# Kernel optimization log

Hardware: AMD Instinct MI355X
Metric: run time of the kernel (lower is better)

Reference implementation:

```python
import jax, jax.numpy as jnp
import numpy as np

N = 16384
D_IN = 1024
HID = [512, 512, 256]
N_PAIRS = 100000
N_CLS = 3


def setup_inputs() -> dict:
    key = jax.random.key(0)
    ks = jax.random.split(key, 16)
    x = jax.random.normal(ks[0], (N, D_IN), dtype=jnp.float32)
    adj = jax.random.uniform(ks[1], (N, N), dtype=jnp.float32) / N  # dense normalized adjacency
    tf_idx = jax.random.randint(ks[2], (N_PAIRS,), 0, N)
    gene_idx = jax.random.randint(ks[3], (N_PAIRS,), 0, N)
    # GCN layer weights
    W0 = jax.random.normal(ks[4], (D_IN, HID[0]), dtype=jnp.float32) / np.sqrt(D_IN)
    b0 = jnp.zeros((HID[0],), dtype=jnp.float32)
    W1 = jax.random.normal(ks[5], (HID[0], HID[1]), dtype=jnp.float32) / np.sqrt(HID[0])
    b1 = jnp.zeros((HID[1],), dtype=jnp.float32)
    W2 = jax.random.normal(ks[6], (HID[1], HID[2]), dtype=jnp.float32) / np.sqrt(HID[1])
    b2 = jnp.zeros((HID[2],), dtype=jnp.float32)
    # MLP head: Linear(2*256 -> 256), GELU, Linear(256 -> 3)
    Wh1 = jax.random.normal(ks[7], (2 * HID[2], HID[2]), dtype=jnp.float32) / np.sqrt(2 * HID[2])
    bh1 = jnp.zeros((HID[2],), dtype=jnp.float32)
    Wh2 = jax.random.normal(ks[8], (HID[2], N_CLS), dtype=jnp.float32) / np.sqrt(HID[2])
    bh2 = jnp.zeros((N_CLS,), dtype=jnp.float32)
    return {"x": x, "adj": adj, "tf_idx": tf_idx, "gene_idx": gene_idx,
            "W0": W0, "b0": b0, "W1": W1, "b1": b1, "W2": W2, "b2": b2,
            "Wh1": Wh1, "bh1": bh1, "Wh2": Wh2, "bh2": bh2}


def reference(x, adj, tf_idx, gene_idx, W0, b0, W1, b1, W2, b2, Wh1, bh1, Wh2, bh2):
    # GCNConv: out = adj @ (x @ W) + b; ReLU between layers (dropout off in eval)
    h = jax.nn.relu(adj @ (x @ W0) + b0)          # [N, 512]
    h = jax.nn.relu(adj @ (h @ W1) + b1)          # [N, 512]
    emb = adj @ (h @ W2) + b2                      # [N, 256]
    pair = jnp.concatenate([emb[tf_idx], emb[gene_idx]], axis=-1)  # [P, 512]
    hdn = jax.nn.gelu(pair @ Wh1 + bh1, approximate=False)          # [P, 256]
    logits = hdn @ Wh2 + bh2                                        # [P, 3]
    return logits
```

## Files before the change

kernel.cpp:

```cpp
#include <hip/hip_runtime.h>
#include <hip/hip_bf16.h>
#include <stdint.h>


using f32x4  = __attribute__((ext_vector_type(4))) float;
using bf16x8 = __attribute__((ext_vector_type(8))) __bf16;
using u16x8  = __attribute__((ext_vector_type(8))) unsigned short;
using u16x4  = __attribute__((ext_vector_type(4))) unsigned short;

static __device__ __forceinline__ unsigned short f2bf(float f) {
  unsigned u = __builtin_bit_cast(unsigned, f);
  u += 0x7FFFu + ((u >> 16) & 1u);
  return (unsigned short)(u >> 16);
}
static __device__ __forceinline__ float bf2f(unsigned short h) {
  unsigned u = ((unsigned)h) << 16;
  return __builtin_bit_cast(float, u);
}
static __device__ __forceinline__ void gload_lds16(const void* g, void* l) {
  __builtin_amdgcn_global_load_lds((__attribute__((address_space(1))) void*)(void*)g,
                                   (__attribute__((address_space(3))) void*)l,
                                   16, 0, 0);
}


__global__ void tcvt_kernel(const float* __restrict__ in,
                            unsigned short* __restrict__ outp, int K, int Nf) {
  int id = blockIdx.x * 256 + threadIdx.x;
  if (id >= K * Nf) return;
  int k = id % K, nf = id / K;
  outp[id] = f2bf(in[(size_t)k * Nf + nf]);
}

__global__ void cvt_bf16_kernel(const float* __restrict__ in,
                                unsigned short* __restrict__ outp, size_t n) {
  size_t i = ((size_t)blockIdx.x * blockDim.x + threadIdx.x) * 8;
  size_t stride = (size_t)gridDim.x * blockDim.x * 8;
  for (; i + 8 <= n; i += stride) {
    const float4* p = (const float4*)(in + i);
    float4 a = p[0], b = p[1];
    u16x8 v;
    v[0] = f2bf(a.x); v[1] = f2bf(a.y); v[2] = f2bf(a.z); v[3] = f2bf(a.w);
    v[4] = f2bf(b.x); v[5] = f2bf(b.y); v[6] = f2bf(b.z); v[7] = f2bf(b.w);
    *(u16x8*)(outp + i) = v;
  }
}

__global__ void reduce2_kernel(const float* __restrict__ Pp, const float* __restrict__ bias,
                               unsigned short* __restrict__ outp, int MN, int Nf) {
  int i = (blockIdx.x * 256 + threadIdx.x) * 4;
  if (i >= MN) return;
  float4 a = *(const float4*)(Pp + i);
  float4 b = *(const float4*)(Pp + MN + i);
  int col = i & (Nf - 1);
  u16x4 o;
  o[0] = f2bf(a.x + b.x + bias[col + 0]);
  o[1] = f2bf(a.y + b.y + bias[col + 1]);
  o[2] = f2bf(a.z + b.z + bias[col + 2]);
  o[3] = f2bf(a.w + b.w + bias[col + 3]);
  *(u16x4*)(outp + i) = o;
}

template <int EP, bool ABF16>
__global__ __launch_bounds__(256, 2)
void gemm_bt(const void* __restrict__ Av, const unsigned short* __restrict__ Bt,
             void* __restrict__ Cout, const float* __restrict__ bias,
             int M, int N, int K, int nbx, int Klen) {
  __shared__ __align__(16) unsigned short As[128 * 64];
  __shared__ __align__(16) unsigned short Bs[128 * 64];
  const int t = threadIdx.x;
  const int l = t & 63;
  const int w = t >> 6;

  int wg = blockIdx.x;
  const int cpx = gridDim.x >> 3;
  wg = (wg & 7) * cpx + (wg >> 3);
  const int mb = wg / nbx, nb = wg % nbx;
  const int kc = blockIdx.y;
  const int koff = kc * Klen;

  const int wr = w >> 1, wc = w & 1;
  f32x4 acc[4][4] = {};

  const int srow = w * 8 + (l >> 3);
  const int sk0  = 8 * ((l & 7) ^ (l >> 3));
  const unsigned short* Bg = Bt + (size_t)(nb * 128 + srow) * K + koff + sk0;
  unsigned short* BsL = Bs + w * 512 + l * 8;
  unsigned short* AsL = As + w * 512 + l * 8;

  const unsigned short* Ag16 = nullptr;
  const float* Ag32 = nullptr;
  unsigned short* AsWr = nullptr;
  int ak = 0, axm = 0;
  if constexpr (ABF16) {
    Ag16 = (const unsigned short*)Av + (size_t)(mb * 128 + srow) * K + koff + sk0;
  } else {
    const int ar = t >> 1;
    ak = (t & 1) * 32;
    axm = (ar & 7) << 3;
    Ag32 = (const float*)Av + (size_t)(mb * 128 + ar) * K + koff + ak;
    AsWr = As + ar * 64;
  }

  const int fr = l & 15, fq = l >> 4;
  const int rxor = (fr & 7) << 3;

  const int steps = Klen >> 6;
  for (int kb = 0; kb < steps; ++kb) {
#pragma unroll
    for (int i = 0; i < 4; ++i)
      gload_lds16(Bg + (size_t)i * 32 * K, BsL + i * 2048);
    Bg += 64;
    if constexpr (ABF16) {
#pragma unroll
      for (int i = 0; i < 4; ++i)
        gload_lds16(Ag16 + (size_t)i * 32 * K, AsL + i * 2048);
      Ag16 += 64;
    } else {
#pragma unroll
      for (int q = 0; q < 4; ++q) {
        float4 c0 = ((const float4*)Ag32)[q * 2];
        float4 c1 = ((const float4*)Ag32)[q * 2 + 1];
        u16x8 v;
        v[0] = f2bf(c0.x); v[1] = f2bf(c0.y); v[2] = f2bf(c0.z); v[3] = f2bf(c0.w);
        v[4] = f2bf(c1.x); v[5] = f2bf(c1.y); v[6] = f2bf(c1.z); v[7] = f2bf(c1.w);
        *(u16x8*)&AsWr[(ak + q * 8) ^ axm] = v;
      }
      Ag32 += 64;
    }
    __syncthreads();

    bf16x8 af[2][4], bfr[2][4];
#pragma unroll
    for (int kk = 0; kk < 2; ++kk) {
#pragma unroll
      for (int mi = 0; mi < 4; ++mi) {
        int arow = wr * 64 + mi * 16 + fr;
        af[kk][mi] = *(const bf16x8*)&As[arow * 64 + ((kk * 32 + fq * 8) ^ rxor)];
      }
#pragma unroll
      for (int ni = 0; ni < 4; ++ni) {
        int brow = wc * 64 + ni * 16 + fr;
        bfr[kk][ni] = *(const bf16x8*)&Bs[brow * 64 + ((kk * 32 + fq * 8) ^ rxor)];
      }
    }
#pragma unroll
    for (int kk = 0; kk < 2; ++kk)
#pragma unroll
      for (int mi = 0; mi < 4; ++mi)
#pragma unroll
        for (int ni = 0; ni < 4; ++ni)
          acc[mi][ni] = __builtin_amdgcn_mfma_f32_16x16x32_bf16(af[kk][mi], bfr[kk][ni],
                                                                acc[mi][ni], 0, 0, 0);
    __syncthreads();
  }

  const int r0 = fq * 4;
  const int c0 = fr;
  const int growb = mb * 128 + wr * 64 + r0;
  const int gcolb = nb * 128 + wc * 64 + c0;
  if constexpr (EP == 0) {
    unsigned short* Ct = (unsigned short*)Cout;
#pragma unroll
    for (int ni = 0; ni < 4; ++ni) {
      int col = gcolb + ni * 16;
#pragma unroll
      for (int mi = 0; mi < 4; ++mi) {
        int row = growb + mi * 16;
        f32x4 v = acc[mi][ni];
        u16x4 o;
        o[0] = f2bf(v[0]); o[1] = f2bf(v[1]); o[2] = f2bf(v[2]); o[3] = f2bf(v[3]);
        *(u16x4*)&Ct[(size_t)col * M + row] = o;
      }
    }
  } else if constexpr (EP == 1) {
    unsigned short* C = (unsigned short*)Cout;
#pragma unroll
    for (int ni = 0; ni < 4; ++ni) {
      int col = gcolb + ni * 16;
      float b = bias[col];
#pragma unroll
      for (int mi = 0; mi < 4; ++mi) {
        int row = growb + mi * 16;
        f32x4 v = acc[mi][ni];
#pragma unroll
        for (int r = 0; r < 4; ++r)
          C[(size_t)(row + r) * N + col] = f2bf(fmaxf(v[r] + b, 0.0f));
      }
    }
  } else {
    float* C = (float*)Cout + (size_t)kc * M * N;
#pragma unroll
    for (int ni = 0; ni < 4; ++ni) {
      int col = gcolb + ni * 16;
#pragma unroll
      for (int mi = 0; mi < 4; ++mi) {
        int row = growb + mi * 16;
        f32x4 v = acc[mi][ni];
#pragma unroll
        for (int r = 0; r < 4; ++r)
          C[(size_t)(row + r) * N + col] = v[r];
      }
    }
  }
}

__global__ __launch_bounds__(256, 2)
void head_kernel(const unsigned short* __restrict__ EMB, const int* __restrict__ tf,
                 const int* __restrict__ gi, const unsigned short* __restrict__ Wh1t,
                 const float* __restrict__ bh1, const float* __restrict__ Wh2,
                 const float* __restrict__ bh2, float* __restrict__ out, int P) {
  __shared__ __align__(16) union SU {
    struct { unsigned short As[64 * 64]; unsigned short Bs[256 * 64]; } s;
    unsigned short hdn[64 * 264];
  } u;
  __shared__ float wh2s[256 * 3];
  const int t = threadIdx.x, l = t & 63, w = t >> 6;
  const int pb = blockIdx.x;

  wh2s[t]       = Wh2[t];
  wh2s[t + 256] = Wh2[t + 256];
  wh2s[t + 512] = Wh2[t + 512];

  const int srow = w * 8 + (l >> 3);
  const int sk0  = 8 * ((l & 7) ^ (l >> 3));
  size_t tfo[2], gio[2];
#pragma unroll
  for (int i = 0; i < 2; ++i) {
    int p = pb * 64 + i * 32 + srow;
    if (p >= P) p = P - 1;
    tfo[i] = (size_t)tf[p] * 256;
    gio[i] = (size_t)gi[p] * 256;
  }
  const unsigned short* BgB = Wh1t + (size_t)srow * 512 + sk0;
  unsigned short* AsL = u.s.As + w * 512 + l * 8;
  unsigned short* BsL = u.s.Bs + w * 512 + l * 8;

  const int fr = l & 15, fq = l >> 4;
  const int rxor = (fr & 7) << 3;

  f32x4 acc[4][4] = {};
  for (int kb = 0; kb < 8; ++kb) {
    const int klo = (kb & 3) * 64 + sk0;
#pragma unroll
    for (int i = 0; i < 2; ++i)
      gload_lds16(EMB + ((kb < 4) ? tfo[i] : gio[i]) + klo, AsL + i * 2048);
#pragma unroll
    for (int i = 0; i < 8; ++i)
      gload_lds16(BgB + (size_t)i * 32 * 512 + kb * 64, BsL + i * 2048);
    __syncthreads();

    bf16x8 af[2][4], bfr[2][4];
#pragma unroll
    for (int kk = 0; kk < 2; ++kk) {
#pragma unroll
      for (int mi = 0; mi < 4; ++mi) {
        int arow = mi * 16 + fr;
        af[kk][mi] = *(const bf16x8*)&u.s.As[arow * 64 + ((kk * 32 + fq * 8) ^ rxor)];
      }
#pragma unroll
      for (int ni = 0; ni < 4; ++ni) {
        int brow = w * 64 + ni * 16 + fr;
        bfr[kk][ni] = *(const bf16x8*)&u.s.Bs[brow * 64 + ((kk * 32 + fq * 8) ^ rxor)];
      }
    }
#pragma unroll
    for (int kk = 0; kk < 2; ++kk)
#pragma unroll
      for (int mi = 0; mi < 4; ++mi)
#pragma unroll
        for (int ni = 0; ni < 4; ++ni)
          acc[mi][ni] = __builtin_amdgcn_mfma_f32_16x16x32_bf16(af[kk][mi], bfr[kk][ni],
                                                                acc[mi][ni], 0, 0, 0);
    __syncthreads();
  }

  const int r0 = fq * 4, c0 = fr;
#pragma unroll
  for (int ni = 0; ni < 4; ++ni) {
    int col = w * 64 + ni * 16 + c0;
    float b = bh1[col];
#pragma unroll
    for (int mi = 0; mi < 4; ++mi) {
      int row = mi * 16 + r0;
      f32x4 v = acc[mi][ni];
#pragma unroll
      for (int r = 0; r < 4; ++r) {
        float xv = v[r] + b;
        float g = 0.5f * xv * (1.0f + erff(xv * 0.70710678118f));
        u.hdn[(row + r) * 264 + col] = f2bf(g);
      }
    }
  }
  __syncthreads();

  const int pl = w * 16 + (l >> 2);
  const int pg = pb * 64 + pl;
  const int ks = (l & 3) * 64;
  float a0 = 0.f, a1 = 0.f, a2 = 0.f;
  const unsigned short* hr = u.hdn + pl * 264 + ks;
#pragma unroll
  for (int kq = 0; kq < 8; ++kq) {
    u16x8 hv = *(const u16x8*)(hr + kq * 8);
#pragma unroll
    for (int j = 0; j < 8; ++j) {
      float h = bf2f(hv[j]);
      int k = ks + kq * 8 + j;
      a0 = fmaf(h, wh2s[k * 3 + 0], a0);
      a1 = fmaf(h, wh2s[k * 3 + 1], a1);
      a2 = fmaf(h, wh2s[k * 3 + 2], a2);
    }
  }
  a0 += __shfl_xor(a0, 1); a0 += __shfl_xor(a0, 2);
  a1 += __shfl_xor(a1, 1); a1 += __shfl_xor(a1, 2);
  a2 += __shfl_xor(a2, 1); a2 += __shfl_xor(a2, 2);
  if ((l & 3) == 0 && pg < P) {
    out[(size_t)pg * 3 + 0] = a0 + bh2[0];
    out[(size_t)pg * 3 + 1] = a1 + bh2[1];
    out[(size_t)pg * 3 + 2] = a2 + bh2[2];
  }
}


extern "C" void kernel_launch(void* const* d_in, const int* in_sizes, int n_in,
                              void* d_out, int out_size, void* d_ws, size_t ws_size,
                              hipStream_t stream) {
  const float* x   = (const float*)d_in[0];
  const float* adj = (const float*)d_in[1];
  const int*   tf  = (const int*)d_in[2];
  const int*   gi  = (const int*)d_in[3];
  const float* W0  = (const float*)d_in[4];
  const float* b0  = (const float*)d_in[5];
  const float* W1  = (const float*)d_in[6];
  const float* b1  = (const float*)d_in[7];
  const float* W2  = (const float*)d_in[8];
  const float* b2  = (const float*)d_in[9];
  const float* Wh1 = (const float*)d_in[10];
  const float* bh1 = (const float*)d_in[11];
  const float* Wh2 = (const float*)d_in[12];
  const float* bh2 = (const float*)d_in[13];
  float* out = (float*)d_out;

  const int NN = 16384;
  const int P = in_sizes[2];

  char* ws = (char*)d_ws;
  size_t off = 0;
  auto alloc = [&](size_t bytes) -> char* {
    char* p = ws + off;
    off += (bytes + 255) & ~(size_t)255;
    return p;
  };
  unsigned short* W0t  = (unsigned short*)alloc((size_t)512 * 1024 * 2);
  unsigned short* W1t  = (unsigned short*)alloc((size_t)512 * 512 * 2);
  unsigned short* W2t  = (unsigned short*)alloc((size_t)256 * 512 * 2);
  unsigned short* Wh1t = (unsigned short*)alloc((size_t)256 * 512 * 2);
  unsigned short* Tt   = (unsigned short*)alloc((size_t)512 * NN * 2);
  unsigned short* H    = (unsigned short*)alloc((size_t)NN * 512 * 2);
  unsigned short* EMB  = (unsigned short*)alloc((size_t)NN * 256 * 2);
  float*          Pp   = (float*)alloc((size_t)2 * NN * 256 * 4);
  size_t base_end = off;

  bool useAdjB = false;
  unsigned short* adjb = nullptr;
  if (ws_size >= base_end + (size_t)NN * NN * 2) {
    adjb = (unsigned short*)alloc((size_t)NN * NN * 2);
    useAdjB = true;
  }

  tcvt_kernel<<<dim3((1024 * 512 + 255) / 256), 256, 0, stream>>>(W0, W0t, 1024, 512);
  tcvt_kernel<<<dim3((512 * 512 + 255) / 256), 256, 0, stream>>>(W1, W1t, 512, 512);
  tcvt_kernel<<<dim3((512 * 256 + 255) / 256), 256, 0, stream>>>(W2, W2t, 512, 256);
  tcvt_kernel<<<dim3((512 * 256 + 255) / 256), 256, 0, stream>>>(Wh1, Wh1t, 512, 256);
  if (useAdjB)
    cvt_bf16_kernel<<<4096, 256, 0, stream>>>(adj, adjb, (size_t)NN * NN);

  gemm_bt<0, false><<<dim3(512), 256, 0, stream>>>(x, W0t, Tt, nullptr,
                                                   NN, 512, 1024, 4, 1024);
  if (useAdjB)
    gemm_bt<1, true><<<dim3(512), 256, 0, stream>>>(adjb, Tt, H, b0,
                                                    NN, 512, NN, 4, NN);
  else
    gemm_bt<1, false><<<dim3(512), 256, 0, stream>>>(adj, Tt, H, b0,
                                                     NN, 512, NN, 4, NN);
  gemm_bt<0, true><<<dim3(512), 256, 0, stream>>>(H, W1t, Tt, nullptr,
                                                  NN, 512, 512, 4, 512);
  if (useAdjB)
    gemm_bt<1, true><<<dim3(512), 256, 0, stream>>>(adjb, Tt, H, b1,
                                                    NN, 512, NN, 4, NN);
  else
    gemm_bt<1, false><<<dim3(512), 256, 0, stream>>>(adj, Tt, H, b1,
                                                     NN, 512, NN, 4, NN);
  gemm_bt<0, true><<<dim3(256), 256, 0, stream>>>(H, W2t, Tt, nullptr,
                                                  NN, 256, 512, 2, 512);
  if (useAdjB)
    gemm_bt<3, true><<<dim3(256, 2), 256, 0, stream>>>(adjb, Tt, Pp, nullptr,
                                                       NN, 256, NN, 2, NN / 2);
  else
    gemm_bt<3, false><<<dim3(256, 2), 256, 0, stream>>>(adj, Tt, Pp, nullptr,
                                                        NN, 256, NN, 2, NN / 2);
  reduce2_kernel<<<dim3(4096), 256, 0, stream>>>(Pp, b2, EMB, NN * 256, 256);
  head_kernel<<<dim3((P + 63) / 64), 256, 0, stream>>>(EMB, tf, gi, Wh1t, bh1,
                                                       Wh2, bh2, out, P);
}
```

Baseline: 1.344 ms.

## Add 256x128-tile 8-wave triple-buffered GEMM for adjacency products

Adds a new GEMM kernel with 512 threads, a 256x128 output tile, and a three-stage LDS ring fed by direct global-to-LDS loads. The loads are split across two half-K MFMA phases and fenced with barriers and priority hints. It replaces the three bf16 adjacency GEMMs, which dominate runtime, to raise reuse of each B tile and to overlap memory traffic with MFMA work. The cost is one block per CU with heavy LDS use (about 144KB), fewer blocks in flight, and scalar per-element epilogue stores.

Measured after the change: 1.380 ms. 2.7% more time.

```diff
diff --git a/kernel.cpp b/kernel.cpp
--- a/kernel.cpp
+++ b/kernel.cpp
@@ -59,6 +59,166 @@
   o[2] = f2bf(a.z + b.z + bias[col + 2]);
   o[3] = f2bf(a.w + b.w + bias[col + 3]);
   *(u16x4*)(outp + i) = o;
+}
+
+template <int EP>
+__global__ __launch_bounds__(512, 1)
+void gemm8p(const unsigned short* __restrict__ A, const unsigned short* __restrict__ Bt,
+            void* __restrict__ Cout, const float* __restrict__ bias,
+            int M, int N, int K, int nbx, int Klen) {
+  __shared__ __align__(16) unsigned short As[3 * 256 * 64];
+  __shared__ __align__(16) unsigned short Bs[3 * 128 * 64];
+  const int t = threadIdx.x, l = t & 63, w = t >> 6;
+
+  int wg = blockIdx.x;
+  const int cpx = gridDim.x >> 3;
+  wg = (wg & 7) * cpx + (wg >> 3);
+  const int mb = wg / nbx, nb = wg % nbx;
+  const int kc = blockIdx.y;
+  const int koff = kc * Klen;
+  const int wr = w >> 1, wc = w & 1;
+  const int fr = l & 15, fq = l >> 4;
+  const int rxor = (fr & 7) << 3;
+
+  float bv[4];
+  if constexpr (EP == 1) {
+#pragma unroll
+    for (int ni = 0; ni < 4; ++ni)
+      bv[ni] = bias[nb * 128 + wc * 64 + ni * 16 + fr];
+  }
+  asm volatile("s_waitcnt vmcnt(0)" ::: "memory");
+  __builtin_amdgcn_sched_barrier(0);
+
+  const int srow = t >> 3;
+  const int sk0  = 8 * ((t & 7) ^ (srow & 7));
+  const unsigned short* Ag = A  + (size_t)(mb * 256 + srow) * K + koff + sk0;
+  const unsigned short* Bg = Bt + (size_t)(nb * 128 + srow) * K + koff + sk0;
+  unsigned short* AsL = As + t * 8;
+  unsigned short* BsL = Bs + t * 8;
+
+  const int NT = Klen >> 6;
+
+#pragma unroll
+  for (int i = 0; i < 4; ++i)
+    gload_lds16(Ag + (size_t)(i * 64) * K, AsL + i * 4096);
+#pragma unroll
+  for (int i = 0; i < 2; ++i)
+    gload_lds16(Bg + (size_t)(i * 64) * K, BsL + i * 4096);
+#pragma unroll
+  for (int i = 0; i < 4; ++i)
+    gload_lds16(Ag + 64 + (size_t)(i * 64) * K, AsL + 16384 + i * 4096);
+#pragma unroll
+  for (int i = 0; i < 2; ++i)
+    gload_lds16(Bg + 64 + (size_t)(i * 64) * K, BsL + 8192 + i * 4096);
+  asm volatile("s_waitcnt vmcnt(6)" ::: "memory");
+  __builtin_amdgcn_sched_barrier(0);
+  __builtin_amdgcn_s_barrier();
+
+  f32x4 acc[4][4] = {};
+  int rb = 0;
+  for (int tt = 0; tt < NT; ++tt) {
+    const int s = tt + 2;
+    const int sb = (rb >= 1) ? rb - 1 : 2;
+    const unsigned short* Ab = As + rb * 16384;
+    const unsigned short* Bb = Bs + rb * 8192;
+    const unsigned short* Ags = Ag + (size_t)s * 64;
+    const unsigned short* Bgs = Bg + (size_t)s * 64;
+    unsigned short* AsS = AsL + sb * 16384;
+    unsigned short* BsS = BsL + sb * 8192;
+
+    bf16x8 a0[4], b0[4];
+#pragma unroll
+    for (int mi = 0; mi < 4; ++mi)
+      a0[mi] = *(const bf16x8*)&Ab[(wr * 64 + mi * 16 + fr) * 64 + ((fq * 8) ^ rxor)];
+#pragma unroll
+    for (int ni = 0; ni < 4; ++ni)
+      b0[ni] = *(const bf16x8*)&Bb[(wc * 64 + ni * 16 + fr) * 64 + ((fq * 8) ^ rxor)];
+    if (s < NT) {
+      gload_lds16(Ags, AsS);
+      gload_lds16(Ags + (size_t)64 * K, AsS + 4096);
+      gload_lds16(Ags + (size_t)128 * K, AsS + 8192);
+    }
+    __builtin_amdgcn_s_barrier();
+    asm volatile("s_waitcnt lgkmcnt(0)" ::: "memory");
+    __builtin_amdgcn_sched_barrier(0);
+    __builtin_amdgcn_s_setprio(1);
+#pragma unroll
+    for (int mi = 0; mi < 4; ++mi)
+#pragma unroll
+      for (int ni = 0; ni < 4; ++ni)
+        acc[mi][ni] = __builtin_amdgcn_mfma_f32_16x16x32_bf16(a0[mi], b0[ni],
+                                                              acc[mi][ni], 0, 0, 0);
+    __builtin_amdgcn_s_setprio(0);
+    __builtin_amdgcn_sched_barrier(0);
+    __builtin_amdgcn_s_barrier();
+
+    bf16x8 a1[4], b1[4];
+#pragma unroll
+    for (int mi = 0; mi < 4; ++mi)
+      a1[mi] = *(const bf16x8*)&Ab[(wr * 64 + mi * 16 + fr) * 64 + ((32 + fq * 8) ^ rxor)];
+#pragma unroll
+    for (int ni = 0; ni < 4; ++ni)
+      b1[ni] = *(const bf16x8*)&Bb[(wc * 64 + ni * 16 + fr) * 64 + ((32 + fq * 8) ^ rxor)];
+    if (s < NT) {
+      gload_lds16(Ags + (size_t)192 * K, AsS + 12288);
+      gload_lds16(Bgs, BsS);
+      gload_lds16(Bgs + (size_t)64 * K, BsS + 4096);
+    }
+    __builtin_amdgcn_s_barrier();
+    asm volatile("s_waitcnt lgkmcnt(0)" ::: "memory");
+    __builtin_amdgcn_sched_barrier(0);
+    __builtin_amdgcn_s_setprio(1);
+#pragma unroll
+    for (int mi = 0; mi < 4; ++mi)
+#pragma unroll
+      for (int ni = 0; ni < 4; ++ni)
+        acc[mi][ni] = __builtin_amdgcn_mfma_f32_16x16x32_bf16(a1[mi], b1[ni],
+                                                              acc[mi][ni], 0, 0, 0);
+    __builtin_amdgcn_s_setprio(0);
+    __builtin_amdgcn_sched_barrier(0);
+
+    if (s < NT) {
+      asm volatile("s_waitcnt vmcnt(6)" ::: "memory");
+    } else {
+      asm volatile("s_waitcnt vmcnt(0)" ::: "memory");
+    }
+    __builtin_amdgcn_sched_barrier(0);
+    __builtin_amdgcn_s_barrier();
+    rb = (rb >= 2) ? 0 : rb + 1;
+  }
+
+  const int r0 = fq * 4;
+  const int growb = mb * 256 + wr * 64 + r0;
+  const int gcolb = nb * 128 + wc * 64 + fr;
+  if constexpr (EP == 1) {
+    unsigned short* C = (unsigned short*)Cout;
+#pragma unroll
+    for (int ni = 0; ni < 4; ++ni) {
+      int col = gcolb + ni * 16;
+#pragma unroll
+      for (int mi = 0; mi < 4; ++mi) {
+        int row = growb + mi * 16;
+        f32x4 v = acc[mi][ni];
+#pragma unroll
+        for (int r = 0; r < 4; ++r)
+          C[(size_t)(row + r) * N + col] = f2bf(fmaxf(v[r] + bv[ni], 0.0f));
+      }
+    }
+  } else {
+    float* C = (float*)Cout + (size_t)kc * M * N;
+#pragma unroll
+    for (int ni = 0; ni < 4; ++ni) {
+      int col = gcolb + ni * 16;
+#pragma unroll
+      for (int mi = 0; mi < 4; ++mi) {
+        int row = growb + mi * 16;
+        f32x4 v = acc[mi][ni];
+#pragma unroll
+        for (int r = 0; r < 4; ++r)
+          C[(size_t)(row + r) * N + col] = v[r];
+      }
+    }
+  }
 }
 
 template <int EP, bool ABF16>
@@ -378,24 +538,22 @@
   gemm_bt<0, false><<<dim3(512), 256, 0, stream>>>(x, W0t, Tt, nullptr,
                                                    NN, 512, 1024, 4, 1024);
   if (useAdjB)
-    gemm_bt<1, true><<<dim3(512), 256, 0, stream>>>(adjb, Tt, H, b0,
-                                                    NN, 512, NN, 4, NN);
+    gemm8p<1><<<dim3(256), 512, 0, stream>>>(adjb, Tt, H, b0, NN, 512, NN, 4, NN);
   else
     gemm_bt<1, false><<<dim3(512), 256, 0, stream>>>(adj, Tt, H, b0,
                                                      NN, 512, NN, 4, NN);
   gemm_bt<0, true><<<dim3(512), 256, 0, stream>>>(H, W1t, Tt, nullptr,
                                                   NN, 512, 512, 4, 512);
   if (useAdjB)
-    gemm_bt<1, true><<<dim3(512), 256, 0, stream>>>(adjb, Tt, H, b1,
-                                                    NN, 512, NN, 4, NN);
+    gemm8p<1><<<dim3(256), 512, 0, stream>>>(adjb, Tt, H, b1, NN, 512, NN, 4, NN);
   else
     gemm_bt<1, false><<<dim3(512), 256, 0, stream>>>(adj, Tt, H, b1,
                                                      NN, 512, NN, 4, NN);
   gemm_bt<0, true><<<dim3(256), 256, 0, stream>>>(H, W2t, Tt, nullptr,
                                                   NN, 256, 512, 2, 512);
   if (useAdjB)
-    gemm_bt<3, true><<<dim3(256, 2), 256, 0, stream>>>(adjb, Tt, Pp, nullptr,
-                                                       NN, 256, NN, 2, NN / 2);
+    gemm8p<3><<<dim3(128, 2), 512, 0, stream>>>(adjb, Tt, Pp, nullptr,
+                                                NN, 256, NN, 2, NN / 2);
   else
     gemm_bt<3, false><<<dim3(256, 2), 256, 0, stream>>>(adj, Tt, Pp, nullptr,
                                                         NN, 256, NN, 2, NN / 2);
```

## Use 256x256-tile split-K GEMM for adjacency products with reduction epilogue

Applied to the files above, without the earlier changes.

Adds a new 512-thread GEMM kernel with 256x256 output tiles and a 4-stage LDS pipeline fed by direct global-to-LDS loads. The three adjacency GEMMs now use it with split-K (2 or 4 partitions), writing fp32 partials that a generalized reduce kernel sums with bias and optional ReLU before converting to bf16. Larger tiles roughly halve the re-reads of the adjacency and feature operands per FLOP. In exchange the code pays extra fp32 partial-sum traffic, one more kernel launch per layer, and a larger workspace.

Result: faster. 1.289 ms (-4.1%).

```diff
diff --git a/kernel.cpp b/kernel.cpp
--- a/kernel.cpp
+++ b/kernel.cpp
@@ -46,19 +46,151 @@
   }
 }
 
-__global__ void reduce2_kernel(const float* __restrict__ Pp, const float* __restrict__ bias,
-                               unsigned short* __restrict__ outp, int MN, int Nf) {
+template <int NPART, bool RELU>
+__global__ void reduceK_kernel(const float* __restrict__ Pp, const float* __restrict__ bias,
+                               unsigned short* __restrict__ outp, int MN, int Nmask) {
   int i = (blockIdx.x * 256 + threadIdx.x) * 4;
   if (i >= MN) return;
-  float4 a = *(const float4*)(Pp + i);
-  float4 b = *(const float4*)(Pp + MN + i);
-  int col = i & (Nf - 1);
+  float4 s = *(const float4*)(Pp + i);
+#pragma unroll
+  for (int p = 1; p < NPART; ++p) {
+    float4 v = *(const float4*)(Pp + (size_t)p * MN + i);
+    s.x += v.x; s.y += v.y; s.z += v.z; s.w += v.w;
+  }
+  int col = i & Nmask;
+  float r0 = s.x + bias[col + 0];
+  float r1 = s.y + bias[col + 1];
+  float r2 = s.z + bias[col + 2];
+  float r3 = s.w + bias[col + 3];
+  if (RELU) {
+    r0 = fmaxf(r0, 0.0f); r1 = fmaxf(r1, 0.0f);
+    r2 = fmaxf(r2, 0.0f); r3 = fmaxf(r3, 0.0f);
+  }
   u16x4 o;
-  o[0] = f2bf(a.x + b.x + bias[col + 0]);
-  o[1] = f2bf(a.y + b.y + bias[col + 1]);
-  o[2] = f2bf(a.z + b.z + bias[col + 2]);
-  o[3] = f2bf(a.w + b.w + bias[col + 3]);
+  o[0] = f2bf(r0); o[1] = f2bf(r1); o[2] = f2bf(r2); o[3] = f2bf(r3);
   *(u16x4*)(outp + i) = o;
+}
+
+__global__ __launch_bounds__(512, 1)
+void gemm256(const unsigned short* __restrict__ A, const unsigned short* __restrict__ Bt,
+             float* __restrict__ Pp, int M, int N, int K, int nbx, int Klen) {
+  __shared__ __align__(16) unsigned short As[4 * 256 * 32];
+  __shared__ __align__(16) unsigned short Bs[4 * 256 * 32];
+  const int t = threadIdx.x, l = t & 63, w = t >> 6;
+
+  int wg = blockIdx.x;
+  const int cpx = gridDim.x >> 3;
+  wg = (wg & 7) * cpx + (wg >> 3);
+  const int mb = wg / nbx, nb = wg % nbx;
+  const int kc = blockIdx.y;
+  const int koff = kc * Klen;
+  const int wr = w >> 2, wc = w & 3;
+  const int fr = l & 15, fq = l >> 4;
+
+  const int srow = t >> 2;
+  const int sk0  = (t & 3) * 8;
+  const unsigned short* AgR = A  + (size_t)(mb * 256 + srow) * K + koff + sk0;
+  const unsigned short* BgR = Bt + (size_t)(nb * 256 + srow) * K + koff + sk0;
+  unsigned short* AsL = As + t * 8;
+  unsigned short* BsL = Bs + t * 8;
+
+  const int NT = Klen >> 5;
+
+#pragma unroll
+  for (int s = 0; s < 3; ++s) {
+    gload_lds16(AgR + s * 32, AsL + s * 8192);
+    gload_lds16(AgR + (size_t)128 * K + s * 32, AsL + s * 8192 + 4096);
+    gload_lds16(BgR + s * 32, BsL + s * 8192);
+    gload_lds16(BgR + (size_t)128 * K + s * 32, BsL + s * 8192 + 4096);
+  }
+  asm volatile("s_waitcnt vmcnt(8)" ::: "memory");
+  __builtin_amdgcn_sched_barrier(0);
+  __builtin_amdgcn_s_barrier();
+
+  f32x4 acc[8][4] = {};
+  for (int tt = 0; tt < NT; ++tt) {
+    const int buf = tt & 3;
+    const int sb  = (tt + 3) & 3;
+    const unsigned short* Ab = As + buf * 8192;
+    const unsigned short* Bb = Bs + buf * 8192;
+    const bool stg = (tt + 3) < NT;
+    const unsigned short* AgS = AgR + (size_t)(tt + 3) * 32;
+    const unsigned short* BgS = BgR + (size_t)(tt + 3) * 32;
+
+    bf16x8 bfr[4], af[4];
+#pragma unroll
+    for (int ni = 0; ni < 4; ++ni)
+      bfr[ni] = *(const bf16x8*)&Bb[(wc * 64 + ni * 16 + fr) * 32 + fq * 8];
+#pragma unroll
+    for (int mi = 0; mi < 4; ++mi)
+      af[mi] = *(const bf16x8*)&Ab[(wr * 128 + mi * 16 + fr) * 32 + fq * 8];
+    if (stg) {
+      gload_lds16(AgS, AsL + sb * 8192);
+      gload_lds16(AgS + (size_t)128 * K, AsL + sb * 8192 + 4096);
+    }
+    __builtin_amdgcn_sched_barrier(0);
+    __builtin_amdgcn_s_barrier();
+    asm volatile("s_waitcnt lgkmcnt(0)" ::: "memory");
+    __builtin_amdgcn_sched_barrier(0);
+    __builtin_amdgcn_s_setprio(1);
+#pragma unroll
+    for (int mi = 0; mi < 4; ++mi)
+#pragma unroll
+      for (int ni = 0; ni < 4; ++ni)
+        acc[mi][ni] = __builtin_amdgcn_mfma_f32_16x16x32_bf16(af[mi], bfr[ni],
+                                                              acc[mi][ni], 0, 0, 0);
+    __builtin_amdgcn_s_setprio(0);
+    __builtin_amdgcn_sched_barrier(0);
+    __builtin_amdgcn_s_barrier();
+
+    bf16x8 ag[4];
+#pragma unroll
+    for (int mi = 0; mi < 4; ++mi)
+      ag[mi] = *(const bf16x8*)&Ab[(wr * 128 + (mi + 4) * 16 + fr) * 32 + fq * 8];
+    if (stg) {
+      gload_lds16(BgS, BsL + sb * 8192);
+      gload_lds16(BgS + (size_t)128 * K, BsL + sb * 8192 + 4096);
+    }
+    __builtin_amdgcn_sched_barrier(0);
+    __builtin_amdgcn_s_barrier();
+    asm volatile("s_waitcnt lgkmcnt(0)" ::: "memory");
+    __builtin_amdgcn_sched_barrier(0);
+    __builtin_amdgcn_s_setprio(1);
+#pragma unroll
+    for (int mi = 0; mi < 4; ++mi)
+#pragma unroll
+      for (int ni = 0; ni < 4; ++ni)
+        acc[mi + 4][ni] = __builtin_amdgcn_mfma_f32_16x16x32_bf16(ag[mi], bfr[ni],
+                                                                  acc[mi + 4][ni], 0, 0, 0);
+    __builtin_amdgcn_s_setprio(0);
+    __builtin_amdgcn_sched_barrier(0);
+
+    if (tt + 4 <= NT) {
+      asm volatile("s_waitcnt vmcnt(8)" ::: "memory");
+    } else if (tt + 3 == NT) {
+      asm volatile("s_waitcnt vmcnt(4)" ::: "memory");
+    } else {
+      asm volatile("s_waitcnt vmcnt(0)" ::: "memory");
+    }
+    __builtin_amdgcn_sched_barrier(0);
+    __builtin_amdgcn_s_barrier();
+  }
+
+  float* C = Pp + (size_t)kc * M * N;
+  const int growb = mb * 256 + wr * 128 + fq * 4;
+  const int gcolb = nb * 256 + wc * 64 + fr;
+#pragma unroll
+  for (int mi = 0; mi < 8; ++mi) {
+    int row = growb + mi * 16;
+#pragma unroll
+    for (int ni = 0; ni < 4; ++ni) {
+      int col = gcolb + ni * 16;
+      f32x4 v = acc[mi][ni];
+#pragma unroll
+      for (int r = 0; r < 4; ++r)
+        C[(size_t)(row + r) * N + col] = v[r];
+    }
+  }
 }
 
 template <int EP, bool ABF16>
@@ -358,7 +490,7 @@
   unsigned short* Tt   = (unsigned short*)alloc((size_t)512 * NN * 2);
   unsigned short* H    = (unsigned short*)alloc((size_t)NN * 512 * 2);
   unsigned short* EMB  = (unsigned short*)alloc((size_t)NN * 256 * 2);
-  float*          Pp   = (float*)alloc((size_t)2 * NN * 256 * 4);
+  float*          Pp   = (float*)alloc((size_t)2 * NN * 512 * 4);
   size_t base_end = off;
 
   bool useAdjB = false;
@@ -377,29 +509,32 @@
 
   gemm_bt<0, false><<<dim3(512), 256, 0, stream>>>(x, W0t, Tt, nullptr,
                                                    NN, 512, 1024, 4, 1024);
-  if (useAdjB)
-    gemm_bt<1, true><<<dim3(512), 256, 0, stream>>>(adjb, Tt, H, b0,
-                                                    NN, 512, NN, 4, NN);
-  else
+  if (useAdjB) {
+    gemm256<<<dim3(128, 2), 512, 0, stream>>>(adjb, Tt, Pp, NN, 512, NN, 2, NN / 2);
+    reduceK_kernel<2, true><<<dim3(8192), 256, 0, stream>>>(Pp, b0, H, NN * 512, 511);
+  } else {
     gemm_bt<1, false><<<dim3(512), 256, 0, stream>>>(adj, Tt, H, b0,
                                                      NN, 512, NN, 4, NN);
+  }
   gemm_bt<0, true><<<dim3(512), 256, 0, stream>>>(H, W1t, Tt, nullptr,
                                                   NN, 512, 512, 4, 512);
-  if (useAdjB)
-    gemm_bt<1, true><<<dim3(512), 256, 0, stream>>>(adjb, Tt, H, b1,
-                                                    NN, 512, NN, 4, NN);
-  else
+  if (useAdjB) {
+    gemm256<<<dim3(128, 2), 512, 0, stream>>>(adjb, Tt, Pp, NN, 512, NN, 2, NN / 2);
+    reduceK_kernel<2, true><<<dim3(8192), 256, 0, stream>>>(Pp, b1, H, NN * 512, 511);
+  } else {
     gemm_bt<1, false><<<dim3(512), 256, 0, stream>>>(adj, Tt, H, b1,
                                                      NN, 512, NN, 4, NN);
+  }
   gemm_bt<0, true><<<dim3(256), 256, 0, stream>>>(H, W2t, Tt, nullptr,
                                                   NN, 256, 512, 2, 512);
-  if (useAdjB)
-    gemm_bt<3, true><<<dim3(256, 2), 256, 0, stream>>>(adjb, Tt, Pp, nullptr,
-                                                       NN, 256, NN, 2, NN / 2);
-  else
+  if (useAdjB) {
+    gemm256<<<dim3(64, 4), 512, 0, stream>>>(adjb, Tt, Pp, NN, 256, NN, 1, NN / 4);
+    reduceK_kernel<4, false><<<dim3(4096), 256, 0, stream>>>(Pp, b2, EMB, NN * 256, 255);
+  } else {
     gemm_bt<3, false><<<dim3(256, 2), 256, 0, stream>>>(adj, Tt, Pp, nullptr,
                                                         NN, 256, NN, 2, NN / 2);
-  reduce2_kernel<<<dim3(4096), 256, 0, stream>>>(Pp, b2, EMB, NN * 256, 256);
+    reduceK_kernel<2, false><<<dim3(4096), 256, 0, stream>>>(Pp, b2, EMB, NN * 256, 255);
+  }
   head_kernel<<<dim3((P + 63) / 64), 256, 0, stream>>>(EMB, tf, gi, Wh1t, bh1,
                                                        Wh2, bh2, out, P);
 }
```
